# Kernel optimization log

Measured on AMD Instinct MI355X. Metric: run time of the kernel, lower is better.

## Reference

```python
import jax, jax.numpy as jnp
import numpy as np

# ---- larq ste_sign: forward = sign (0 -> +1), backward = clipped straight-through ----
def _sign(x):
    return jnp.where(x >= 0, jnp.ones_like(x), -jnp.ones_like(x))

@jax.custom_vjp
def ste_sign(x):
    return _sign(x)

def _ste_fwd(x):
    return _sign(x), x

def _ste_bwd(x, g):
    return (g * (jnp.abs(x) <= 1.0).astype(g.dtype),)

ste_sign.defvjp(_ste_fwd, _ste_bwd)

BN_EPS = 1e-3  # keras BatchNormalization default epsilon

def conv2d(x, w, padding):
    # x: NHWC, w: HWIO
    return jax.lax.conv_general_dilated(
        x, w, window_strides=(1, 1), padding=padding,
        dimension_numbers=('NHWC', 'HWIO', 'NHWC'))

def maxpool2(x):
    return jax.lax.reduce_window(x, -jnp.inf, jax.lax.max,
                                 (1, 2, 2, 1), (1, 2, 2, 1), 'VALID')

def batchnorm(x, mean, var, beta):
    # BatchNormalization(scale=False): gamma fixed at 1
    return (x - mean) * jax.lax.rsqrt(var + BN_EPS) + beta


def setup_inputs() -> dict:
    key = jax.random.key(0)
    ks = jax.random.split(key, 20)
    d = {}
    d['x'] = jax.random.normal(ks[0], (64, 128, 128, 3), dtype=jnp.float32)
    d['w1'] = jax.random.normal(ks[1], (3, 3, 3, 32), dtype=jnp.float32)
    d['m1'] = jax.random.normal(ks[2], (32,), dtype=jnp.float32)
    d['v1'] = jax.random.uniform(ks[3], (32,), dtype=jnp.float32)
    d['b1'] = jax.random.normal(ks[4], (32,), dtype=jnp.float32)
    d['w2'] = jax.random.normal(ks[5], (3, 3, 32, 64), dtype=jnp.float32)
    d['m2'] = jax.random.normal(ks[6], (64,), dtype=jnp.float32)
    d['v2'] = jax.random.uniform(ks[7], (64,), dtype=jnp.float32)
    d['b2'] = jax.random.normal(ks[8], (64,), dtype=jnp.float32)
    d['w3'] = jax.random.normal(ks[9], (3, 3, 64, 128), dtype=jnp.float32)
    d['m3'] = jax.random.normal(ks[10], (128,), dtype=jnp.float32)
    d['v3'] = jax.random.uniform(ks[11], (128,), dtype=jnp.float32)
    d['b3'] = jax.random.normal(ks[12], (128,), dtype=jnp.float32)
    d['w4'] = jax.random.normal(ks[13], (3, 3, 128, 256), dtype=jnp.float32)
    d['m4'] = jax.random.normal(ks[14], (256,), dtype=jnp.float32)
    d['v4'] = jax.random.uniform(ks[15], (256,), dtype=jnp.float32)
    d['b4'] = jax.random.normal(ks[16], (256,), dtype=jnp.float32)
    return d


def reference(x, w1, m1, v1, b1, w2, m2, v2, b2, w3, m3, v3, b3, w4, m4, v4, b4):
    # Stem: QuantConv2D(32,3x3,valid) with kernel quantized only (no input quantizer)
    y = conv2d(x, ste_sign(w1), 'VALID')          # [B,126,126,32]
    y = batchnorm(maxpool2(y), m1, v1, b1)        # [B,63,63,32]
    # Three binarized blocks: ste_sign(input) conv ste_sign(kernel), same padding
    for w, m, v, b in ((w2, m2, v2, b2), (w3, m3, v3, b3), (w4, m4, v4, b4)):
        y = conv2d(ste_sign(y), ste_sign(w), 'SAME')
        y = batchnorm(maxpool2(y), m, v, b)       # halves spatial dims
    return y                                      # [B,7,7,256]
```

## Files before the change

### kernel.cpp

```cpp
#include <hip/hip_runtime.h>
#include <stdint.h>

#define BN_EPS 1e-3f

template <int CIN, int COUT>
__device__ inline void packw(const float* __restrict__ w, uint32_t* __restrict__ wp, int idx) {
    const int CINW = CIN / 32;
    int co = idx % COUT;
    int t2 = idx / COUT;
    int wi = t2 % CINW;
    int tap = t2 / CINW;
    uint32_t word = 0;
#pragma unroll
    for (int bb = 0; bb < 32; bb++) {
        float val = w[((tap * CIN) + wi * 32 + bb) * COUT + co];
        word |= (uint32_t)(val < 0.f) << bb;
    }
    wp[idx] = word;
}

__global__ void pack_all(const float* __restrict__ w1, const float* __restrict__ w2,
                         const float* __restrict__ w3, const float* __restrict__ w4,
                         float* __restrict__ w1s, uint32_t* __restrict__ w2p,
                         uint32_t* __restrict__ w3p, uint32_t* __restrict__ w4p) {
    int idx = blockIdx.x * 256 + threadIdx.x;
    if (idx < 864) {
        w1s[idx] = (w1[idx] < 0.f) ? -1.f : 1.f;
        return;
    }
    idx -= 864;
    if (idx < 576) { packw<32, 64>(w2, w2p, idx); return; }
    idx -= 576;
    if (idx < 2304) { packw<64, 128>(w3, w3p, idx); return; }
    idx -= 2304;
    if (idx < 9216) { packw<128, 256>(w4, w4p, idx); return; }
}

__global__ __launch_bounds__(256, 4) void conv1_k(const float* __restrict__ x,
                                                  const float* __restrict__ w1s,
                                                  const float* __restrict__ m1,
                                                  const float* __restrict__ v1,
                                                  const float* __restrict__ b1,
                                                  uint32_t* __restrict__ y1p) {
    __shared__ __align__(16) float xt[34 * 104];

    int tile = blockIdx.x;
    int tx = tile & 3;
    int ty = (tile >> 2) & 3;
    int n  = tile >> 4;
    int ph0 = ty * 16, pw0 = tx * 16;
    int r0 = 2 * ph0;
    int cf0 = pw0 * 6;

    for (int i = threadIdx.x; i < 34 * 102; i += 256) {
        int r = i / 102, c = i % 102;
        int gr = r0 + r, gcf = cf0 + c;
        float vv = 0.f;
        if (gr < 128 && gcf < 384)
            vv = x[(size_t)(n * 128 + gr) * 384 + gcf];
        xt[r * 104 + c] = vv;
    }

    __syncthreads();

    int wave = threadIdx.x >> 6, lane = threadIdx.x & 63;
    int px = lane & 15, py = (wave << 2) + (lane >> 4);
    int ph = ph0 + py, pw = pw0 + px;

    float win[48];
#pragma unroll
    for (int r = 0; r < 4; r++) {
        const float2* bp = (const float2*)&xt[(2 * py + r) * 104 + 6 * px];
#pragma unroll
        for (int q = 0; q < 6; q++) {
            float2 f2 = bp[q];
            win[r * 12 + 2 * q]     = f2.x;
            win[r * 12 + 2 * q + 1] = f2.y;
        }
    }

    uint32_t word = 0;
#pragma unroll 1
    for (int cg = 0; cg < 4; cg++) {
        float acc[8][4];
#pragma unroll
        for (int j = 0; j < 8; j++)
#pragma unroll
            for (int p = 0; p < 4; p++) acc[j][p] = 0.f;

        const float* sgc = w1s + cg * 8;
#pragma unroll
        for (int kh = 0; kh < 3; kh++)
#pragma unroll
            for (int kw = 0; kw < 3; kw++)
#pragma unroll
                for (int ci = 0; ci < 3; ci++) {
                    int tap = (kh * 3 + kw) * 3 + ci;
                    float x00 = win[kh * 12 + kw * 3 + ci];
                    float x01 = win[kh * 12 + (kw + 1) * 3 + ci];
                    float x10 = win[(kh + 1) * 12 + kw * 3 + ci];
                    float x11 = win[(kh + 1) * 12 + (kw + 1) * 3 + ci];
                    float4 s0 = *(const float4*)(sgc + tap * 32);
                    float4 s1 = *(const float4*)(sgc + tap * 32 + 4);
                    float sv[8] = {s0.x, s0.y, s0.z, s0.w, s1.x, s1.y, s1.z, s1.w};
#pragma unroll
                    for (int j = 0; j < 8; j++) {
                        acc[j][0] += x00 * sv[j];
                        acc[j][1] += x01 * sv[j];
                        acc[j][2] += x10 * sv[j];
                        acc[j][3] += x11 * sv[j];
                    }
                }
#pragma unroll
        for (int j = 0; j < 8; j++) {
            float mx = fmaxf(fmaxf(acc[j][0], acc[j][1]), fmaxf(acc[j][2], acc[j][3]));
            int ch = cg * 8 + j;
            float y = (mx - m1[ch]) * rsqrtf(v1[ch] + BN_EPS) + b1[ch];
            word |= (uint32_t)(y < 0.f) << ch;
        }
    }

    if (ph < 63 && pw < 63)
        y1p[(n * 63 + ph) * 63 + pw] = word;
}

__global__ __launch_bounds__(256) void bconv2(const uint32_t* __restrict__ y1p,
                                              const uint32_t* __restrict__ w2p,
                                              const float* __restrict__ m,
                                              const float* __restrict__ v,
                                              const float* __restrict__ b,
                                              uint2* __restrict__ y2p) {
    int gw = __builtin_amdgcn_readfirstlane(blockIdx.x * 4 + (threadIdx.x >> 6));
    int lane = threadIdx.x & 63;
    int pwg = gw & 7;
    int t = gw >> 3;
    int ph = t % 31;
    int n = t / 31;

    uint32_t wq[9];
#pragma unroll
    for (int tap = 0; tap < 9; tap++) wq[tap] = w2p[tap * 64 + lane];
    float mm = m[lane], vv = v[lane], bb = b[lane];

    uint2 o0, o1, o2, o3;

    if (ph > 0 && pwg > 0) {
        int row0 = 2 * ph - 1, col0 = 8 * pwg - 1;
        uint32_t win[4][10];
#pragma unroll
        for (int r = 0; r < 4; r++)
#pragma unroll
            for (int c = 0; c < 10; c++)
                win[r][c] = y1p[(n * 63 + row0 + r) * 63 + min(col0 + c, 62)];

        uint2 res[4];
#pragma unroll
        for (int p = 0; p < 4; p++) {
            int a0 = 0, a1 = 0, a2 = 0, a3 = 0;
#pragma unroll
            for (int kh = 0; kh < 3; kh++)
#pragma unroll
                for (int kw = 0; kw < 3; kw++) {
                    uint32_t w = wq[kh * 3 + kw];
                    a0 += __popc(win[kh][2 * p + kw] ^ w);
                    a1 += __popc(win[kh][2 * p + kw + 1] ^ w);
                    a2 += __popc(win[kh + 1][2 * p + kw] ^ w);
                    a3 += __popc(win[kh + 1][2 * p + kw + 1] ^ w);
                }
            int mn = min(min(a0, a1), min(a2, a3));
            int best = 288 - 2 * mn;
            float y = ((float)best - mm) * rsqrtf(vv + BN_EPS) + bb;
            unsigned long long bal = __ballot(y < 0.f);
            res[p] = make_uint2((uint32_t)bal, (uint32_t)(bal >> 32));
        }
        o0 = res[0]; o1 = res[1]; o2 = res[2]; o3 = res[3];
    } else {
        uint2 res[4];
#pragma unroll
        for (int p = 0; p < 4; p++) {
            int pw = 4 * pwg + p;
            int best = -1000000;
            if (pw < 31) {
#pragma unroll
                for (int dy = 0; dy < 2; dy++)
#pragma unroll
                    for (int dx = 0; dx < 2; dx++) {
                        int oh = 2 * ph + dy, ow = 2 * pw + dx;
                        int acc = 0, K = 0;
                        for (int kh = 0; kh < 3; kh++) {
                            int ih = oh - 1 + kh;
                            if (ih < 0 || ih >= 63) continue;
                            for (int kw = 0; kw < 3; kw++) {
                                int iw = ow - 1 + kw;
                                if (iw < 0 || iw >= 63) continue;
                                acc += __popc(y1p[(n * 63 + ih) * 63 + iw] ^ wq[kh * 3 + kw]);
                                K += 32;
                            }
                        }
                        best = max(best, K - 2 * acc);
                    }
            }
            float y = ((float)best - mm) * rsqrtf(vv + BN_EPS) + bb;
            unsigned long long bal = __ballot(y < 0.f);
            res[p] = make_uint2((uint32_t)bal, (uint32_t)(bal >> 32));
        }
        o0 = res[0]; o1 = res[1]; o2 = res[2]; o3 = res[3];
    }

    uint2 rr = o0;
    if (lane == 1) rr = o1;
    if (lane == 2) rr = o2;
    if (lane == 3) rr = o3;
    int pws = 4 * pwg + lane;
    if (lane < 4 && pws < 31)
        y2p[(n * 31 + ph) * 31 + pws] = rr;
}

__global__ __launch_bounds__(256) void bconv3(const uint2* __restrict__ y2p,
                                              const uint32_t* __restrict__ w3p,
                                              const float* __restrict__ m,
                                              const float* __restrict__ v,
                                              const float* __restrict__ b,
                                              uint32_t* __restrict__ y3p) {
    int gw = __builtin_amdgcn_readfirstlane(blockIdx.x * 4 + (threadIdx.x >> 6));
    int lane = threadIdx.x & 63;
    int half = gw & 1;
    int t = gw >> 1;
    int pwg = t & 7;
    t >>= 3;
    int ph = t % 15;
    int n = t / 15;
    int co = half * 64 + lane;

    uint32_t wq0[9], wq1[9];
#pragma unroll
    for (int tap = 0; tap < 9; tap++) {
        wq0[tap] = w3p[(tap * 2 + 0) * 128 + co];
        wq1[tap] = w3p[(tap * 2 + 1) * 128 + co];
    }
    float mm = m[co], vv = v[co], bb = b[co];

    unsigned long long bal0, bal1;

    if (ph > 0 && pwg > 0) {
        int row0 = 2 * ph - 1, col0 = 4 * pwg - 1;
        uint2 win[4][6];
#pragma unroll
        for (int r = 0; r < 4; r++)
#pragma unroll
            for (int c = 0; c < 6; c++)
                win[r][c] = y2p[(n * 31 + row0 + r) * 31 + min(col0 + c, 30)];

        unsigned long long bals[2];
#pragma unroll
        for (int p = 0; p < 2; p++) {
            int a0 = 0, a1 = 0, a2 = 0, a3 = 0;
#pragma unroll
            for (int kh = 0; kh < 3; kh++)
#pragma unroll
                for (int kw = 0; kw < 3; kw++) {
                    int tap = kh * 3 + kw;
                    uint32_t u0 = wq0[tap], u1 = wq1[tap];
                    a0 += __popc(win[kh][2 * p + kw].x ^ u0) + __popc(win[kh][2 * p + kw].y ^ u1);
                    a1 += __popc(win[kh][2 * p + kw + 1].x ^ u0) + __popc(win[kh][2 * p + kw + 1].y ^ u1);
                    a2 += __popc(win[kh + 1][2 * p + kw].x ^ u0) + __popc(win[kh + 1][2 * p + kw].y ^ u1);
                    a3 += __popc(win[kh + 1][2 * p + kw + 1].x ^ u0) + __popc(win[kh + 1][2 * p + kw + 1].y ^ u1);
                }
            int mn = min(min(a0, a1), min(a2, a3));
            int best = 576 - 2 * mn;
            float y = ((float)best - mm) * rsqrtf(vv + BN_EPS) + bb;
            bals[p] = __ballot(y < 0.f);
        }
        bal0 = bals[0]; bal1 = bals[1];
    } else {
        unsigned long long bals[2];
#pragma unroll
        for (int p = 0; p < 2; p++) {
            int pw = 2 * pwg + p;
            int best = -1000000;
            if (pw < 15) {
#pragma unroll
                for (int dy = 0; dy < 2; dy++)
#pragma unroll
                    for (int dx = 0; dx < 2; dx++) {
                        int oh = 2 * ph + dy, ow = 2 * pw + dx;
                        int acc = 0, K = 0;
                        for (int kh = 0; kh < 3; kh++) {
                            int ih = oh - 1 + kh;
                            if (ih < 0 || ih >= 31) continue;
                            for (int kw = 0; kw < 3; kw++) {
                                int iw = ow - 1 + kw;
                                if (iw < 0 || iw >= 31) continue;
                                uint2 iv = y2p[(n * 31 + ih) * 31 + iw];
                                int tap = kh * 3 + kw;
                                acc += __popc(iv.x ^ wq0[tap]) + __popc(iv.y ^ wq1[tap]);
                                K += 64;
                            }
                        }
                        best = max(best, K - 2 * acc);
                    }
            }
            float y = ((float)best - mm) * rsqrtf(vv + BN_EPS) + bb;
            bals[p] = __ballot(y < 0.f);
        }
        bal0 = bals[0]; bal1 = bals[1];
    }

    uint32_t val = (uint32_t)bal0;
    if (lane == 1) val = (uint32_t)(bal0 >> 32);
    if (lane == 2) val = (uint32_t)bal1;
    if (lane == 3) val = (uint32_t)(bal1 >> 32);
    int p = lane >> 1;
    int pw = 2 * pwg + p;
    if (lane < 4 && pw < 15) {
        int pixel = (n * 15 + ph) * 15 + pw;
        y3p[pixel * 4 + half * 2 + (lane & 1)] = val;
    }
}

__global__ __launch_bounds__(256) void bconv4(const uint4* __restrict__ y3p,
                                              const uint32_t* __restrict__ w4p,
                                              const float* __restrict__ m,
                                              const float* __restrict__ v,
                                              const float* __restrict__ b,
                                              float* __restrict__ out) {
    int pixel = blockIdx.x;
    int lane = threadIdx.x & 63;
    int co = (threadIdx.x >> 6) * 64 + lane;
    int pw = pixel % 7;
    int t = pixel / 7;
    int ph = t % 7;
    int n = t / 7;

    uint4 wq[9];
#pragma unroll
    for (int tap = 0; tap < 9; tap++) {
        wq[tap].x = w4p[(tap * 4 + 0) * 256 + co];
        wq[tap].y = w4p[(tap * 4 + 1) * 256 + co];
        wq[tap].z = w4p[(tap * 4 + 2) * 256 + co];
        wq[tap].w = w4p[(tap * 4 + 3) * 256 + co];
    }

    int best;
    if (ph > 0 && pw > 0) {
        const uint4* p = y3p + (n * 15 + (2 * ph - 1)) * 15 + (2 * pw - 1);
        int a0 = 0, a1 = 0, a2 = 0, a3 = 0;
#pragma unroll
        for (int r = 0; r < 4; r++)
#pragma unroll
            for (int c = 0; c < 4; c++) {
                uint4 iv = p[r * 15 + c];
#pragma unroll
                for (int kh = 0; kh < 3; kh++) {
                    int dy = r - kh;
                    if (dy < 0 || dy > 1) continue;
#pragma unroll
                    for (int kw = 0; kw < 3; kw++) {
                        int dx = c - kw;
                        if (dx < 0 || dx > 1) continue;
                        int tap = kh * 3 + kw;
                        int pc = __popc(iv.x ^ wq[tap].x) + __popc(iv.y ^ wq[tap].y)
                               + __popc(iv.z ^ wq[tap].z) + __popc(iv.w ^ wq[tap].w);
                        if (dy == 0 && dx == 0) a0 += pc;
                        else if (dy == 0) a1 += pc;
                        else if (dx == 0) a2 += pc;
                        else a3 += pc;
                    }
                }
            }
        best = max(max(1152 - 2 * a0, 1152 - 2 * a1), max(1152 - 2 * a2, 1152 - 2 * a3));
    } else {
        best = -1000000;
#pragma unroll
        for (int dy = 0; dy < 2; dy++)
#pragma unroll
            for (int dx = 0; dx < 2; dx++) {
                int oh = 2 * ph + dy, ow = 2 * pw + dx;
                int acc = 0, K = 0;
                for (int kh = 0; kh < 3; kh++) {
                    int ih = oh - 1 + kh;
                    if (ih < 0 || ih >= 15) continue;
                    for (int kw = 0; kw < 3; kw++) {
                        int iw = ow - 1 + kw;
                        if (iw < 0 || iw >= 15) continue;
                        uint4 iv = y3p[(n * 15 + ih) * 15 + iw];
                        int tap = kh * 3 + kw;
                        acc += __popc(iv.x ^ wq[tap].x) + __popc(iv.y ^ wq[tap].y)
                             + __popc(iv.z ^ wq[tap].z) + __popc(iv.w ^ wq[tap].w);
                        K += 128;
                    }
                }
                best = max(best, K - 2 * acc);
            }
    }
    float y = ((float)best - m[co]) * rsqrtf(v[co] + BN_EPS) + b[co];
    out[pixel * 256 + co] = y;
}

extern "C" void kernel_launch(void* const* d_in, const int* in_sizes, int n_in,
                              void* d_out, int out_size, void* d_ws, size_t ws_size,
                              hipStream_t stream) {
    const float* x  = (const float*)d_in[0];
    const float* w1 = (const float*)d_in[1];
    const float* m1 = (const float*)d_in[2];
    const float* v1 = (const float*)d_in[3];
    const float* b1 = (const float*)d_in[4];
    const float* w2 = (const float*)d_in[5];
    const float* m2 = (const float*)d_in[6];
    const float* v2 = (const float*)d_in[7];
    const float* b2 = (const float*)d_in[8];
    const float* w3 = (const float*)d_in[9];
    const float* m3 = (const float*)d_in[10];
    const float* v3 = (const float*)d_in[11];
    const float* b3 = (const float*)d_in[12];
    const float* w4 = (const float*)d_in[13];
    const float* m4 = (const float*)d_in[14];
    const float* v4 = (const float*)d_in[15];
    const float* b4 = (const float*)d_in[16];
    float* out = (float*)d_out;

    char* ws = (char*)d_ws;
    size_t off = 0;
    auto take = [&](size_t bytes) -> char* {
        char* p = ws + off;
        off += (bytes + 255) & ~(size_t)255;
        return p;
    };
    uint32_t* y1p = (uint32_t*)take((size_t)64 * 63 * 63 * 4);
    uint2*    y2p = (uint2*)take((size_t)64 * 31 * 31 * 8);
    uint32_t* y3p = (uint32_t*)take((size_t)64 * 15 * 15 * 16);
    float*    w1s = (float*)take(864 * 4);
    uint32_t* w2p = (uint32_t*)take(576 * 4);
    uint32_t* w3p = (uint32_t*)take(2304 * 4);
    uint32_t* w4p = (uint32_t*)take(9216 * 4);

    pack_all<<<(864 + 576 + 2304 + 9216 + 255) / 256, 256, 0, stream>>>(
        w1, w2, w3, w4, w1s, w2p, w3p, w4p);

    conv1_k<<<64 * 16, 256, 0, stream>>>(x, w1s, m1, v1, b1, y1p);

    bconv2<<<(64 * 31 * 8) / 4, 256, 0, stream>>>(y1p, w2p, m2, v2, b2, y2p);

    bconv3<<<(64 * 15 * 8 * 2) / 4, 256, 0, stream>>>(y2p, w3p, m3, v3, b3, y3p);

    bconv4<<<64 * 7 * 7, 256, 0, stream>>>((const uint4*)y3p, w4p, m4, v4, b4, out);
}
```

Baseline: 171.2 us.

## Stage input rows in LDS for binary conv layers and remap blocks per row

bconv2 and bconv3 now assign one block per (batch, output row), cooperatively load the 4 needed input rows into shared memory, and have each wave loop over several column groups reading windows from LDS instead of global memory. bconv4 stages its 4x4 packed input patch in shared memory once per block rather than each wave reading it from global. The per-channel rsqrt is hoisted out of the loops. This cuts redundant global/L2 loads of overlapping windows, at the cost of a __syncthreads, fewer blocks, and more serial work per wave.

```diff
diff --git a/kernel.cpp b/kernel.cpp
--- a/kernel.cpp
+++ b/kernel.cpp
@@ -130,90 +130,100 @@
                                               const float* __restrict__ v,
                                               const float* __restrict__ b,
                                               uint2* __restrict__ y2p) {
-    int gw = __builtin_amdgcn_readfirstlane(blockIdx.x * 4 + (threadIdx.x >> 6));
+    __shared__ uint32_t tile[4 * 64];
+
+    int blk = blockIdx.x;
+    int ph = blk % 31;
+    int n  = blk / 31;
     int lane = threadIdx.x & 63;
-    int pwg = gw & 7;
-    int t = gw >> 3;
-    int ph = t % 31;
-    int n = t / 31;
+    int wave = __builtin_amdgcn_readfirstlane(threadIdx.x >> 6);
+
+    if (ph > 0) {
+        int row0 = 2 * ph - 1;
+        for (int i = threadIdx.x; i < 4 * 63; i += 256) {
+            int r = i / 63, c = i % 63;
+            tile[r * 64 + c] = y1p[(n * 63 + row0 + r) * 63 + c];
+        }
+    }
+    __syncthreads();
 
     uint32_t wq[9];
 #pragma unroll
     for (int tap = 0; tap < 9; tap++) wq[tap] = w2p[tap * 64 + lane];
     float mm = m[lane], vv = v[lane], bb = b[lane];
-
-    uint2 o0, o1, o2, o3;
-
-    if (ph > 0 && pwg > 0) {
-        int row0 = 2 * ph - 1, col0 = 8 * pwg - 1;
-        uint32_t win[4][10];
-#pragma unroll
-        for (int r = 0; r < 4; r++)
-#pragma unroll
-            for (int c = 0; c < 10; c++)
-                win[r][c] = y1p[(n * 63 + row0 + r) * 63 + min(col0 + c, 62)];
-
+    float rs = rsqrtf(vv + BN_EPS);
+
+    for (int it = 0; it < 2; it++) {
+        int pwg = wave * 2 + it;
         uint2 res[4];
-#pragma unroll
-        for (int p = 0; p < 4; p++) {
-            int a0 = 0, a1 = 0, a2 = 0, a3 = 0;
-#pragma unroll
-            for (int kh = 0; kh < 3; kh++)
-#pragma unroll
-                for (int kw = 0; kw < 3; kw++) {
-                    uint32_t w = wq[kh * 3 + kw];
-                    a0 += __popc(win[kh][2 * p + kw] ^ w);
-                    a1 += __popc(win[kh][2 * p + kw + 1] ^ w);
-                    a2 += __popc(win[kh + 1][2 * p + kw] ^ w);
-                    a3 += __popc(win[kh + 1][2 * p + kw + 1] ^ w);
+
+        if (ph > 0 && pwg > 0) {
+            int col0 = 8 * pwg - 1;
+            uint32_t win[4][10];
+#pragma unroll
+            for (int r = 0; r < 4; r++)
+#pragma unroll
+                for (int c = 0; c < 10; c++)
+                    win[r][c] = tile[r * 64 + min(col0 + c, 62)];
+
+#pragma unroll
+            for (int p = 0; p < 4; p++) {
+                int a0 = 0, a1 = 0, a2 = 0, a3 = 0;
+#pragma unroll
+                for (int kh = 0; kh < 3; kh++)
+#pragma unroll
+                    for (int kw = 0; kw < 3; kw++) {
+                        uint32_t w = wq[kh * 3 + kw];
+                        a0 += __popc(win[kh][2 * p + kw] ^ w);
+                        a1 += __popc(win[kh][2 * p + kw + 1] ^ w);
+                        a2 += __popc(win[kh + 1][2 * p + kw] ^ w);
+                        a3 += __popc(win[kh + 1][2 * p + kw + 1] ^ w);
+                    }
+                int mn = min(min(a0, a1), min(a2, a3));
+                int best = 288 - 2 * mn;
+                float y = ((float)best - mm) * rs + bb;
+                unsigned long long bal = __ballot(y < 0.f);
+                res[p] = make_uint2((uint32_t)bal, (uint32_t)(bal >> 32));
+            }
+        } else {
+#pragma unroll
+            for (int p = 0; p < 4; p++) {
+                int pw = 4 * pwg + p;
+                int best = -1000000;
+                if (pw < 31) {
+#pragma unroll
+                    for (int dy = 0; dy < 2; dy++)
+#pragma unroll
+                        for (int dx = 0; dx < 2; dx++) {
+                            int oh = 2 * ph + dy, ow = 2 * pw + dx;
+                            int acc = 0, K = 0;
+                            for (int kh = 0; kh < 3; kh++) {
+                                int ih = oh - 1 + kh;
+                                if (ih < 0 || ih >= 63) continue;
+                                for (int kw = 0; kw < 3; kw++) {
+                                    int iw = ow - 1 + kw;
+                                    if (iw < 0 || iw >= 63) continue;
+                                    acc += __popc(y1p[(n * 63 + ih) * 63 + iw] ^ wq[kh * 3 + kw]);
+                                    K += 32;
+                                }
+                            }
+                            best = max(best, K - 2 * acc);
+                        }
                 }
-            int mn = min(min(a0, a1), min(a2, a3));
-            int best = 288 - 2 * mn;
-            float y = ((float)best - mm) * rsqrtf(vv + BN_EPS) + bb;
-            unsigned long long bal = __ballot(y < 0.f);
-            res[p] = make_uint2((uint32_t)bal, (uint32_t)(bal >> 32));
-        }
-        o0 = res[0]; o1 = res[1]; o2 = res[2]; o3 = res[3];
-    } else {
-        uint2 res[4];
-#pragma unroll
-        for (int p = 0; p < 4; p++) {
-            int pw = 4 * pwg + p;
-            int best = -1000000;
-            if (pw < 31) {
-#pragma unroll
-                for (int dy = 0; dy < 2; dy++)
-#pragma unroll
-                    for (int dx = 0; dx < 2; dx++) {
-                        int oh = 2 * ph + dy, ow = 2 * pw + dx;
-                        int acc = 0, K = 0;
-                        for (int kh = 0; kh < 3; kh++) {
-                            int ih = oh - 1 + kh;
-                            if (ih < 0 || ih >= 63) continue;
-                            for (int kw = 0; kw < 3; kw++) {
-                                int iw = ow - 1 + kw;
-                                if (iw < 0 || iw >= 63) continue;
-                                acc += __popc(y1p[(n * 63 + ih) * 63 + iw] ^ wq[kh * 3 + kw]);
-                                K += 32;
-                            }
-                        }
-                        best = max(best, K - 2 * acc);
-                    }
-            }
-            float y = ((float)best - mm) * rsqrtf(vv + BN_EPS) + bb;
-            unsigned long long bal = __ballot(y < 0.f);
-            res[p] = make_uint2((uint32_t)bal, (uint32_t)(bal >> 32));
-        }
-        o0 = res[0]; o1 = res[1]; o2 = res[2]; o3 = res[3];
-    }
-
-    uint2 rr = o0;
-    if (lane == 1) rr = o1;
-    if (lane == 2) rr = o2;
-    if (lane == 3) rr = o3;
-    int pws = 4 * pwg + lane;
-    if (lane < 4 && pws < 31)
-        y2p[(n * 31 + ph) * 31 + pws] = rr;
+                float y = ((float)best - mm) * rs + bb;
+                unsigned long long bal = __ballot(y < 0.f);
+                res[p] = make_uint2((uint32_t)bal, (uint32_t)(bal >> 32));
+            }
+        }
+
+        uint2 rr = res[0];
+        if (lane == 1) rr = res[1];
+        if (lane == 2) rr = res[2];
+        if (lane == 3) rr = res[3];
+        int pws = 4 * pwg + lane;
+        if (lane < 4 && pws < 31)
+            y2p[(n * 31 + ph) * 31 + pws] = rr;
+    }
 }
 
 __global__ __launch_bounds__(256) void bconv3(const uint2* __restrict__ y2p,
@@ -222,15 +232,24 @@
                                               const float* __restrict__ v,
                                               const float* __restrict__ b,
                                               uint32_t* __restrict__ y3p) {
-    int gw = __builtin_amdgcn_readfirstlane(blockIdx.x * 4 + (threadIdx.x >> 6));
+    __shared__ uint2 tile[4 * 32];
+
+    int blk = blockIdx.x;
+    int ph = blk % 15;
+    int n  = blk / 15;
     int lane = threadIdx.x & 63;
-    int half = gw & 1;
-    int t = gw >> 1;
-    int pwg = t & 7;
-    t >>= 3;
-    int ph = t % 15;
-    int n = t / 15;
+    int wave = __builtin_amdgcn_readfirstlane(threadIdx.x >> 6);
+    int half = wave & 1;
     int co = half * 64 + lane;
+
+    if (ph > 0) {
+        int row0 = 2 * ph - 1;
+        for (int i = threadIdx.x; i < 4 * 31; i += 256) {
+            int r = i / 31, c = i % 31;
+            tile[r * 32 + c] = y2p[(n * 31 + row0 + r) * 31 + c];
+        }
+    }
+    __syncthreads();
 
     uint32_t wq0[9], wq1[9];
 #pragma unroll
@@ -239,82 +258,86 @@
         wq1[tap] = w3p[(tap * 2 + 1) * 128 + co];
     }
     float mm = m[co], vv = v[co], bb = b[co];
-
-    unsigned long long bal0, bal1;
-
-    if (ph > 0 && pwg > 0) {
-        int row0 = 2 * ph - 1, col0 = 4 * pwg - 1;
-        uint2 win[4][6];
-#pragma unroll
-        for (int r = 0; r < 4; r++)
-#pragma unroll
-            for (int c = 0; c < 6; c++)
-                win[r][c] = y2p[(n * 31 + row0 + r) * 31 + min(col0 + c, 30)];
-
-        unsigned long long bals[2];
-#pragma unroll
-        for (int p = 0; p < 2; p++) {
-            int a0 = 0, a1 = 0, a2 = 0, a3 = 0;
-#pragma unroll
-            for (int kh = 0; kh < 3; kh++)
-#pragma unroll
-                for (int kw = 0; kw < 3; kw++) {
-                    int tap = kh * 3 + kw;
-                    uint32_t u0 = wq0[tap], u1 = wq1[tap];
-                    a0 += __popc(win[kh][2 * p + kw].x ^ u0) + __popc(win[kh][2 * p + kw].y ^ u1);
-                    a1 += __popc(win[kh][2 * p + kw + 1].x ^ u0) + __popc(win[kh][2 * p + kw + 1].y ^ u1);
-                    a2 += __popc(win[kh + 1][2 * p + kw].x ^ u0) + __popc(win[kh + 1][2 * p + kw].y ^ u1);
-                    a3 += __popc(win[kh + 1][2 * p + kw + 1].x ^ u0) + __popc(win[kh + 1][2 * p + kw + 1].y ^ u1);
+    float rs = rsqrtf(vv + BN_EPS);
+
+    for (int it = 0; it < 4; it++) {
+        int pwg = (wave >> 1) * 4 + it;
+        unsigned long long bal0, bal1;
+
+        if (ph > 0 && pwg > 0) {
+            int col0 = 4 * pwg - 1;
+            uint2 win[4][6];
+#pragma unroll
+            for (int r = 0; r < 4; r++)
+#pragma unroll
+                for (int c = 0; c < 6; c++)
+                    win[r][c] = tile[r * 32 + min(col0 + c, 30)];
+
+            unsigned long long bals[2];
+#pragma unroll
+            for (int p = 0; p < 2; p++) {
+                int a0 = 0, a1 = 0, a2 = 0, a3 = 0;
+#pragma unroll
+                for (int kh = 0; kh < 3; kh++)
+#pragma unroll
+                    for (int kw = 0; kw < 3; kw++) {
+                        int tap = kh * 3 + kw;
+                        uint32_t u0 = wq0[tap], u1 = wq1[tap];
+                        a0 += __popc(win[kh][2 * p + kw].x ^ u0) + __popc(win[kh][2 * p + kw].y ^ u1);
+                        a1 += __popc(win[kh][2 * p + kw + 1].x ^ u0) + __popc(win[kh][2 * p + kw + 1].y ^ u1);
+                        a2 += __popc(win[kh + 1][2 * p + kw].x ^ u0) + __popc(win[kh + 1][2 * p + kw].y ^ u1);
+                        a3 += __popc(win[kh + 1][2 * p + kw + 1].x ^ u0) + __popc(win[kh + 1][2 * p + kw + 1].y ^ u1);
+                    }
+                int mn = min(min(a0, a1), min(a2, a3));
+                int best = 576 - 2 * mn;
+                float y = ((float)best - mm) * rs + bb;
+                bals[p] = __ballot(y < 0.f);
+            }
+            bal0 = bals[0]; bal1 = bals[1];
+        } else {
+            unsigned long long bals[2];
+#pragma unroll
+            for (int p = 0; p < 2; p++) {
+                int pw = 2 * pwg + p;
+                int best = -1000000;
+                if (pw < 15) {
+#pragma unroll
+                    for (int dy = 0; dy < 2; dy++)
+#pragma unroll
+                        for (int dx = 0; dx < 2; dx++) {
+                            int oh = 2 * ph + dy, ow = 2 * pw + dx;
+                            int acc = 0, K = 0;
+                            for (int kh = 0; kh < 3; kh++) {
+                                int ih = oh - 1 + kh;
+                                if (ih < 0 || ih >= 31) continue;
+                                for (int kw = 0; kw < 3; kw++) {
+                                    int iw = ow - 1 + kw;
+                                    if (iw < 0 || iw >= 31) continue;
+                                    uint2 iv = y2p[(n * 31 + ih) * 31 + iw];
+                                    int tap = kh * 3 + kw;
+                                    acc += __popc(iv.x ^ wq0[tap]) + __popc(iv.y ^ wq1[tap]);
+                                    K += 64;
+                                }
+                            }
+                            best = max(best, K - 2 * acc);
+                        }
                 }
-            int mn = min(min(a0, a1), min(a2, a3));
-            int best = 576 - 2 * mn;
-            float y = ((float)best - mm) * rsqrtf(vv + BN_EPS) + bb;
-            bals[p] = __ballot(y < 0.f);
-        }
-        bal0 = bals[0]; bal1 = bals[1];
-    } else {
-        unsigned long long bals[2];
-#pragma unroll
-        for (int p = 0; p < 2; p++) {
-            int pw = 2 * pwg + p;
-            int best = -1000000;
-            if (pw < 15) {
-#pragma unroll
-                for (int dy = 0; dy < 2; dy++)
-#pragma unroll
-                    for (int dx = 0; dx < 2; dx++) {
-                        int oh = 2 * ph + dy, ow = 2 * pw + dx;
-                        int acc = 0, K = 0;
-                        for (int kh = 0; kh < 3; kh++) {
-                            int ih = oh - 1 + kh;
-                            if (ih < 0 || ih >= 31) continue;
-                            for (int kw = 0; kw < 3; kw++) {
-                                int iw = ow - 1 + kw;
-                                if (iw < 0 || iw >= 31) continue;
-                                uint2 iv = y2p[(n * 31 + ih) * 31 + iw];
-                                int tap = kh * 3 + kw;
-                                acc += __popc(iv.x ^ wq0[tap]) + __popc(iv.y ^ wq1[tap]);
-                                K += 64;
-                            }
-                        }
-                        best = max(best, K - 2 * acc);
-                    }
-            }
-            float y = ((float)best - mm) * rsqrtf(vv + BN_EPS) + bb;
-            bals[p] = __ballot(y < 0.f);
-        }
-        bal0 = bals[0]; bal1 = bals[1];
-    }
-
-    uint32_t val = (uint32_t)bal0;
-    if (lane == 1) val = (uint32_t)(bal0 >> 32);
-    if (lane == 2) val = (uint32_t)bal1;
-    if (lane == 3) val = (uint32_t)(bal1 >> 32);
-    int p = lane >> 1;
-    int pw = 2 * pwg + p;
-    if (lane < 4 && pw < 15) {
-        int pixel = (n * 15 + ph) * 15 + pw;
-        y3p[pixel * 4 + half * 2 + (lane & 1)] = val;
+                float y = ((float)best - mm) * rs + bb;
+                bals[p] = __ballot(y < 0.f);
+            }
+            bal0 = bals[0]; bal1 = bals[1];
+        }
+
+        uint32_t val = (uint32_t)bal0;
+        if (lane == 1) val = (uint32_t)(bal0 >> 32);
+        if (lane == 2) val = (uint32_t)bal1;
+        if (lane == 3) val = (uint32_t)(bal1 >> 32);
+        int p = lane >> 1;
+        int pw = 2 * pwg + p;
+        if (lane < 4 && pw < 15) {
+            int pixel = (n * 15 + ph) * 15 + pw;
+            y3p[pixel * 4 + half * 2 + (lane & 1)] = val;
+        }
     }
 }
 
@@ -324,6 +347,8 @@
                                               const float* __restrict__ v,
                                               const float* __restrict__ b,
                                               float* __restrict__ out) {
+    __shared__ __align__(16) uint32_t tile[64];
+
     int pixel = blockIdx.x;
     int lane = threadIdx.x & 63;
     int co = (threadIdx.x >> 6) * 64 + lane;
@@ -332,6 +357,19 @@
     int ph = t % 7;
     int n = t / 7;
 
+    if (threadIdx.x < 64) {
+        int tt = threadIdx.x;
+        int r = tt >> 4, e = (tt >> 2) & 3, w = tt & 3;
+        int gr = 2 * ph - 1 + r, gc = 2 * pw - 1 + e;
+        uint32_t val = 0;
+        if (gr >= 0 && gr < 15 && gc >= 0 && gc < 15)
+            val = ((const uint32_t*)y3p)[(((size_t)(n * 15 + gr) * 15 + gc) << 2) + w];
+        tile[tt] = val;
+    }
+    __syncthreads();
+
+    const uint4* tp = (const uint4*)tile;
+
     uint4 wq[9];
 #pragma unroll
     for (int tap = 0; tap < 9; tap++) {
@@ -343,13 +381,12 @@
 
     int best;
     if (ph > 0 && pw > 0) {
-        const uint4* p = y3p + (n * 15 + (2 * ph - 1)) * 15 + (2 * pw - 1);
         int a0 = 0, a1 = 0, a2 = 0, a3 = 0;
 #pragma unroll
         for (int r = 0; r < 4; r++)
 #pragma unroll
             for (int c = 0; c < 4; c++) {
-                uint4 iv = p[r * 15 + c];
+                uint4 iv = tp[r * 4 + c];
 #pragma unroll
                 for (int kh = 0; kh < 3; kh++) {
                     int dy = r - kh;
@@ -377,13 +414,15 @@
             for (int dx = 0; dx < 2; dx++) {
                 int oh = 2 * ph + dy, ow = 2 * pw + dx;
                 int acc = 0, K = 0;
+#pragma unroll
                 for (int kh = 0; kh < 3; kh++) {
                     int ih = oh - 1 + kh;
                     if (ih < 0 || ih >= 15) continue;
+#pragma unroll
                     for (int kw = 0; kw < 3; kw++) {
                         int iw = ow - 1 + kw;
                         if (iw < 0 || iw >= 15) continue;
-                        uint4 iv = y3p[(n * 15 + ih) * 15 + iw];
+                        uint4 iv = tp[(dy + kh) * 4 + (dx + kw)];
                         int tap = kh * 3 + kw;
                         acc += __popc(iv.x ^ wq[tap].x) + __popc(iv.y ^ wq[tap].y)
                              + __popc(iv.z ^ wq[tap].z) + __popc(iv.w ^ wq[tap].w);
@@ -439,9 +478,9 @@
 
     conv1_k<<<64 * 16, 256, 0, stream>>>(x, w1s, m1, v1, b1, y1p);
 
-    bconv2<<<(64 * 31 * 8) / 4, 256, 0, stream>>>(y1p, w2p, m2, v2, b2, y2p);
-
-    bconv3<<<(64 * 15 * 8 * 2) / 4, 256, 0, stream>>>(y2p, w3p, m3, v3, b3, y3p);
+    bconv2<<<64 * 31, 256, 0, stream>>>(y1p, w2p, m2, v2, b2, y2p);
+
+    bconv3<<<64 * 15, 256, 0, stream>>>(y2p, w3p, m3, v3, b3, y3p);
 
     bconv4<<<64 * 7 * 7, 256, 0, stream>>>((const uint4*)y3p, w4p, m4, v4, b4, out);
 }
```

Result: slower. 202.6 us (+18.3%).
